# Kernel tuning notes

Measured on AMD Instinct MI355X. Metric: run time of the kernel, lower is better.

Reference implementation:

```python
import jax, jax.numpy as jnp
import numpy as np

GRID = 48
F = GRID * GRID        # number of mesh faces
C = 128                # channels
H = 8                  # attention heads
DH = C // H
B = 2                  # meshes in batch
WID = 256              # SelectionPrediction width


def _bfs_levels():
    """BFS flood-fill levels on a 4-connected GRIDxGRID face graph, anchor at center.
    Returns [n_levels, max_ring] int32, padded with F (dropped on scatter)."""
    c = GRID // 2
    ii, jj = np.meshgrid(np.arange(GRID), np.arange(GRID), indexing='ij')
    d = (np.abs(ii - c) + np.abs(jj - c)).reshape(-1)  # BFS depth == Manhattan dist
    L = int(d.max()) + 1
    Bd = int(np.bincount(d).max())
    idx = np.full((L, Bd), F, dtype=np.int32)
    for lv in range(L):
        faces = np.nonzero(d == lv)[0]
        idx[lv, :faces.size] = faces
    return jnp.asarray(idx)


def setup_inputs() -> dict:
    key = jax.random.key(0)
    ks = jax.random.split(key, 16)
    s = 1.0 / np.sqrt(C)
    sw = 1.0 / np.sqrt(WID)
    return {
        'x':  jax.random.normal(ks[0], (B, C, F), jnp.float32),
        # AnchorAttentionBlock projections (q/k/v/out)
        'Wq': jax.random.normal(ks[1], (C, C), jnp.float32) * s,
        'Wk': jax.random.normal(ks[2], (C, C), jnp.float32) * s,
        'Wv': jax.random.normal(ks[3], (C, C), jnp.float32) * s,
        'Wo': jax.random.normal(ks[4], (C, C), jnp.float32) * s,
        # SelectionPrediction (n_input=C, width=256, depth=3, sigmoid)
        'W1': jax.random.normal(ks[5], (C, WID), jnp.float32) * s,
        'b1': jnp.zeros((WID,), jnp.float32),
        'W2': jax.random.normal(ks[6], (WID, WID), jnp.float32) * sw,
        'b2': jnp.zeros((WID,), jnp.float32),
        'W3': jax.random.normal(ks[7], (WID, WID), jnp.float32) * sw,
        'b3': jnp.zeros((WID,), jnp.float32),
        'W4': jax.random.normal(ks[8], (WID, WID), jnp.float32) * sw,
        'b4': jnp.zeros((WID,), jnp.float32),
        'W5': jax.random.normal(ks[9], (WID, 1), jnp.float32) * sw,
        'b5': jnp.zeros((1,), jnp.float32),
        'levels_idx': _bfs_levels(),
    }


def reference(x, Wq, Wk, Wv, Wo, W1, b1, W2, b2, W3, b3, W4, b4, W5, b5, levels_idx):
    scale = 1.0 / jnp.sqrt(jnp.asarray(DH, x.dtype))

    def flood(feats):                       # feats: [F, C], one mesh
        def step(cur, idx):                 # idx: [Bd] boundary ring (pad = F)
            q = cur[idx]                                    # [Bd, C] (pad rows clamp-gather)
            qh = (q @ Wq).reshape(-1, H, DH)                # [Bd, H, DH]
            kh = (cur @ Wk).reshape(F, H, DH)               # global fftype: keys = all faces
            vh = (cur @ Wv).reshape(F, H, DH)
            att = jax.nn.softmax(jnp.einsum('bhd,fhd->bhf', qh, kh) * scale, axis=-1)
            o = jnp.einsum('bhf,fhd->bhd', att, vh).reshape(-1, C) @ Wo
            new = q + o                                     # mode='resid'
            return cur.at[idx].set(new, mode='drop'), None  # pad idx == F -> dropped
        out, _ = jax.lax.scan(step, feats, levels_idx)
        return out

    final = jax.vmap(flood)(x.transpose(0, 2, 1))           # [B, F, C]
    # SelectionPrediction on final_features.transpose(2,1)
    h = jax.nn.relu(final @ W1 + b1)
    h = jax.nn.relu(h @ W2 + b2)
    h = jax.nn.relu(h @ W3 + b3)
    h = jax.nn.relu(h @ W4 + b4)
    scores = jax.nn.sigmoid(h @ W5 + b5)                    # [B, F, 1] in [0, 1]
    return final.transpose(0, 2, 1), scores
```

## Files before the change

### kernel.cpp

```cpp
#include <hip/hip_runtime.h>
#include <hip/hip_bf16.h>
#include <stdint.h>

#define GRIDN 48
#define F 2304
#define C 128
#define H 8
#define DH 16
#define NB 2
#define WID 256
#define NLV 49
#define SMH (H * 18)
#define GLV 7

typedef __hip_bfloat16 bf16;

__device__ __forceinline__ float b2f(bf16 v) { return __bfloat162float(v); }

__global__ void k_permdetect(const void* __restrict__ x, int* __restrict__ flag,
                             int* __restrict__ permIdx, int* __restrict__ lvflags) {
    __shared__ int cnt[NLV], start[NLV];
    __shared__ int bad;
    int t = threadIdx.x;
    if (t == 0) bad = 0;
    if (t < NLV) cnt[t] = 0;
    for (int i = t; i < 2 * NLV; i += 256) lvflags[i] = 0;
    __syncthreads();
    {
        const bf16* xb = (const bf16*)x;
        int insane = 0;
        #pragma unroll
        for (int i = 0; i < 8; ++i) {
            float v = b2f(xb[t * 8 + i]);
            if (!(fabsf(v) < 1e10f)) insane = 1;
        }
        if (insane) atomicOr(&bad, 1);
    }
    for (int f = t; f < F; f += 256) {
        int d = abs(f / GRIDN - GRIDN / 2) + abs(f % GRIDN - GRIDN / 2);
        atomicAdd(&cnt[d], 1);
    }
    __syncthreads();
    if (t == 0) {
        int s = 0;
        for (int l = 0; l < NLV; ++l) { start[l] = s; s += cnt[l]; }
        *flag = bad;
    }
    __syncthreads();
    for (int f = t; f < F; f += 256) {
        int d = abs(f / GRIDN - GRIDN / 2) + abs(f % GRIDN - GRIDN / 2);
        permIdx[f] = atomicAdd(&start[d], 1);
    }
}

struct WSeg { const void* src; int off; int cnt; };
struct WSegs { WSeg s[14]; };

__global__ void k_convert(WSegs segs, const int* __restrict__ flag,
                          float* __restrict__ dst, int total) {
    int i = blockIdx.x * blockDim.x + threadIdx.x;
    if (i >= total) return;
    bool f32 = (*flag != 0);
    #pragma unroll 1
    for (int j = 0; j < 14; ++j) {
        int off = segs.s[j].off, cnt = segs.s[j].cnt;
        if (i >= off && i < off + cnt) {
            int k = i - off;
            dst[i] = f32 ? ((const float*)segs.s[j].src)[k]
                         : b2f(((const bf16*)segs.s[j].src)[k]);
            return;
        }
    }
}

__global__ void k_transpose_in(const void* __restrict__ x, const int* __restrict__ flag,
                               float* __restrict__ cur) {
    __shared__ float tile[32][33];
    bool f32 = (*flag != 0);
    int b = blockIdx.z;
    int f0 = blockIdx.x * 32, c0 = blockIdx.y * 32;
    int tx = threadIdx.x, ty = threadIdx.y;
    #pragma unroll
    for (int i = 0; i < 4; ++i) {
        int c = c0 + ty + i * 8;
        size_t idx = ((size_t)b * C + c) * F + f0 + tx;
        tile[ty + i * 8][tx] = f32 ? ((const float*)x)[idx] : b2f(((const bf16*)x)[idx]);
    }
    __syncthreads();
    #pragma unroll
    for (int i = 0; i < 4; ++i) {
        int f = f0 + ty + i * 8;
        cur[((size_t)b * F + f) * C + c0 + tx] = tile[tx][ty + i * 8];
    }
}

__global__ __launch_bounds__(128) void k_proj_init(
        const float* __restrict__ cur, const int* __restrict__ permIdx,
        const float* __restrict__ Wq, const float* __restrict__ Wk, const float* __restrict__ Wv,
        float* __restrict__ qh, float* __restrict__ khT, float* __restrict__ vhT) {
    __shared__ float rows[8][C];
    int r0 = blockIdx.x * 8;
    int tid = threadIdx.x;
    #pragma unroll
    for (int r = 0; r < 8; ++r) rows[r][tid] = cur[(size_t)(r0 + r) * C + tid];
    __syncthreads();
    float aq[8], ak[8], av[8];
    #pragma unroll
    for (int r = 0; r < 8; ++r) { aq[r] = 0.f; ak[r] = 0.f; av[r] = 0.f; }
    for (int k = 0; k < C; ++k) {
        float wq = Wq[k * C + tid];
        float wk = Wk[k * C + tid];
        float wv = Wv[k * C + tid];
        #pragma unroll
        for (int r = 0; r < 8; ++r) {
            float xv = rows[r][k];
            aq[r] = fmaf(xv, wq, aq[r]);
            ak[r] = fmaf(xv, wk, ak[r]);
            av[r] = fmaf(xv, wv, av[r]);
        }
    }
    const float scale = 0.25f;
    #pragma unroll
    for (int r = 0; r < 8; ++r) {
        int grow = r0 + r;
        int mesh = grow / F, face = grow % F;
        int p = permIdx[face];
        qh[(size_t)grow * C + tid] = aq[r] * scale;
        khT[((size_t)mesh * C + tid) * F + p] = ak[r];
        vhT[((size_t)mesh * C + tid) * F + p] = av[r];
    }
}

struct Rings { int v[NLV + 1]; };
struct Pairs { int v[NLV + 1]; };

__global__ __launch_bounds__(256) void k_static(
        int Bd, Rings rings, Pairs pairs,
        const int* __restrict__ levels,
        const float* __restrict__ qh_all,
        const float* __restrict__ khT, const float* __restrict__ vhT,
        float* __restrict__ smS) {
    int bx = blockIdx.x;
    int mesh = bx & 1;
    int gp = bx >> 1;
    int lv = 0;
    while (gp >= pairs.v[lv + 1]) ++lv;
    int spair = gp - pairs.v[lv];
    int rs = rings.v[lv];
    int s0 = spair * 2, s1 = s0 + 1;
    int face0 = (s0 < Bd) ? levels[lv * Bd + s0] : F;
    int face1 = (s1 < Bd) ? levels[lv * Bd + s1] : F;
    bool a0 = (face0 >= 0 && face0 < F), a1 = (face1 >= 0 && face1 < F);
    if (!a0 && !a1) return;

    __shared__ float sQh[2][C];
    int tid = threadIdx.x;
    size_t row0 = ((size_t)mesh * F + face0) * C;
    size_t row1 = ((size_t)mesh * F + face1) * C;
    if (tid < C) sQh[0][tid] = a0 ? qh_all[row0 + tid] : 0.f;
    else { int c = tid - C; sQh[1][c] = a1 ? qh_all[row1 + c] : 0.f; }
    __syncthreads();

    int head = tid >> 5, sub = tid & 31;
    float q0[DH], q1[DH];
    #pragma unroll
    for (int d = 0; d < DH; ++d) { q0[d] = sQh[0][head * DH + d]; q1[d] = sQh[1][head * DH + d]; }

    const float* Kb = khT + ((size_t)mesh * C + head * DH) * F;
    const float* Vb = vhT + ((size_t)mesh * C + head * DH) * F;

    float m0 = -1e30f, l0 = 0.f, m1 = -1e30f, l1 = 0.f;
    float acc0[DH], acc1[DH];
    #pragma unroll
    for (int d = 0; d < DH; ++d) { acc0[d] = 0.f; acc1[d] = 0.f; }

    int base0 = rs & ~127;
    for (int base = base0; base < F; base += 128) {
        int p4 = base + 4 * sub;
        float sx0 = 0, sy0 = 0, sz0 = 0, sw0 = 0;
        float sx1 = 0, sy1 = 0, sz1 = 0, sw1 = 0;
        #pragma unroll
        for (int d = 0; d < DH; ++d) {
            float4 kk = *(const float4*)(Kb + d * F + p4);
            float a = q0[d], b = q1[d];
            sx0 = fmaf(a, kk.x, sx0); sy0 = fmaf(a, kk.y, sy0);
            sz0 = fmaf(a, kk.z, sz0); sw0 = fmaf(a, kk.w, sw0);
            sx1 = fmaf(b, kk.x, sx1); sy1 = fmaf(b, kk.y, sy1);
            sz1 = fmaf(b, kk.z, sz1); sw1 = fmaf(b, kk.w, sw1);
        }
        float g0 = 1.f, g1 = 1.f, g2 = 1.f, g3 = 1.f;
        if (base < rs) {
            g0 = (p4     >= rs) ? 1.f : 0.f; g1 = (p4 + 1 >= rs) ? 1.f : 0.f;
            g2 = (p4 + 2 >= rs) ? 1.f : 0.f; g3 = (p4 + 3 >= rs) ? 1.f : 0.f;
        }
        float mx0 = fmaxf(fmaxf(sx0, sy0), fmaxf(sz0, sw0));
        float mn0 = fmaxf(m0, mx0);
        float c0 = __expf(m0 - mn0);
        float px0 = __expf(sx0 - mn0) * g0, py0 = __expf(sy0 - mn0) * g1;
        float pz0 = __expf(sz0 - mn0) * g2, pw0 = __expf(sw0 - mn0) * g3;
        l0 = fmaf(l0, c0, px0 + py0 + pz0 + pw0);
        m0 = mn0;
        float mx1 = fmaxf(fmaxf(sx1, sy1), fmaxf(sz1, sw1));
        float mn1 = fmaxf(m1, mx1);
        float c1e = __expf(m1 - mn1);
        float px1 = __expf(sx1 - mn1) * g0, py1 = __expf(sy1 - mn1) * g1;
        float pz1 = __expf(sz1 - mn1) * g2, pw1 = __expf(sw1 - mn1) * g3;
        l1 = fmaf(l1, c1e, px1 + py1 + pz1 + pw1);
        m1 = mn1;
        #pragma unroll
        for (int d = 0; d < DH; ++d) {
            float4 vv = *(const float4*)(Vb + d * F + p4);
            float w0 = fmaf(px0, vv.x, fmaf(py0, vv.y, fmaf(pz0, vv.z, pw0 * vv.w)));
            float w1 = fmaf(px1, vv.x, fmaf(py1, vv.y, fmaf(pz1, vv.z, pw1 * vv.w)));
            acc0[d] = fmaf(acc0[d], c0, w0);
            acc1[d] = fmaf(acc1[d], c1e, w1);
        }
    }

    #pragma unroll
    for (int w = 16; w >= 1; w >>= 1) {
        float mo = __shfl_xor(m0, w), lo = __shfl_xor(l0, w);
        float mn = fmaxf(m0, mo);
        float ca = __expf(m0 - mn), cb = __expf(mo - mn);
        l0 = l0 * ca + lo * cb;
        #pragma unroll
        for (int d = 0; d < DH; ++d) {
            float ao = __shfl_xor(acc0[d], w);
            acc0[d] = acc0[d] * ca + ao * cb;
        }
        m0 = mn;
        mo = __shfl_xor(m1, w); lo = __shfl_xor(l1, w);
        mn = fmaxf(m1, mo);
        ca = __expf(m1 - mn); cb = __expf(mo - mn);
        l1 = l1 * ca + lo * cb;
        #pragma unroll
        for (int d = 0; d < DH; ++d) {
            float ao = __shfl_xor(acc1[d], w);
            acc1[d] = acc1[d] * ca + ao * cb;
        }
        m1 = mn;
    }
    if (sub == 0) {
        if (a0) {
            float* S = smS + (size_t)(mesh * F + face0) * SMH + head * 18;
            S[0] = m0; S[1] = l0;
            #pragma unroll
            for (int d = 0; d < DH; ++d) S[2 + d] = acc0[d];
        }
        if (a1) {
            float* S = smS + (size_t)(mesh * F + face1) * SMH + head * 18;
            S[0] = m1; S[1] = l1;
            #pragma unroll
            for (int d = 0; d < DH; ++d) S[2 + d] = acc1[d];
        }
    }
}

struct Grp { int lv0; int rs0; int bofs[GLV + 1]; int rs[GLV]; int re[GLV]; int ns[GLV]; };

__global__ __launch_bounds__(256, 3) void k_group(
        int Bd, Grp grp,
        const int* __restrict__ levels, const int* __restrict__ permIdx,
        const float* __restrict__ qh_all, float* __restrict__ cur,
        float* __restrict__ khT, float* __restrict__ vhT,
        const float* __restrict__ smS,
        const float* __restrict__ Wk, const float* __restrict__ Wv,
        const float* __restrict__ Wo,
        float* __restrict__ stgK, float* __restrict__ stgV,
        int* __restrict__ lvflags) {
    int bx = blockIdx.x;
    int g = 0;
    while (bx >= grp.bofs[g + 1]) ++g;
    int lb = bx - grp.bofs[g];
    int mesh = lb & 1;
    int spair = lb >> 1;
    int lv = grp.lv0 + g;
    int rs0 = grp.rs0;

    int s0 = spair * 2, s1 = s0 + 1;
    int face0 = (s0 < Bd) ? levels[lv * Bd + s0] : F;
    int face1 = (s1 < Bd) ? levels[lv * Bd + s1] : F;
    bool a0 = (face0 >= 0 && face0 < F), a1 = (face1 >= 0 && face1 < F);

    __shared__ float sQh[2][C], sQ[2][C], sRed[2][C], sNew[C];
    __shared__ float sL[2][H];
    int tid = threadIdx.x;
    size_t row0 = ((size_t)mesh * F + face0) * C;
    size_t row1 = ((size_t)mesh * F + face1) * C;
    if (tid < C) {
        if (a0) { sQ[0][tid] = cur[row0 + tid]; sQh[0][tid] = qh_all[row0 + tid]; }
        else    { sQ[0][tid] = 0.f; sQh[0][tid] = 0.f; }
    } else {
        int c = tid - C;
        if (a1) { sQ[1][c] = cur[row1 + c]; sQh[1][c] = qh_all[row1 + c]; }
        else    { sQ[1][c] = 0.f; sQh[1][c] = 0.f; }
    }
    __syncthreads();

    int head = tid >> 5, sub = tid & 31;
    float q0[DH], q1[DH];
    #pragma unroll
    for (int d = 0; d < DH; ++d) { q0[d] = sQh[0][head * DH + d]; q1[d] = sQh[1][head * DH + d]; }

    const float* Kb = khT + ((size_t)mesh * C + head * DH) * F;
    const float* Vb = vhT + ((size_t)mesh * C + head * DH) * F;

    float m0 = -1e30f, l0 = 0.f, m1 = -1e30f, l1 = 0.f;
    float acc0[DH], acc1[DH];
    #pragma unroll
    for (int d = 0; d < DH; ++d) { acc0[d] = 0.f; acc1[d] = 0.f; }

    for (int base = 0; base < rs0; base += 128) {
        int p4 = base + 4 * sub;
        float sx0 = 0, sy0 = 0, sz0 = 0, sw0 = 0;
        float sx1 = 0, sy1 = 0, sz1 = 0, sw1 = 0;
        #pragma unroll
        for (int d = 0; d < DH; ++d) {
            float4 kk = *(const float4*)(Kb + d * F + p4);
            float a = q0[d], b = q1[d];
            sx0 = fmaf(a, kk.x, sx0); sy0 = fmaf(a, kk.y, sy0);
            sz0 = fmaf(a, kk.z, sz0); sw0 = fmaf(a, kk.w, sw0);
            sx1 = fmaf(b, kk.x, sx1); sy1 = fmaf(b, kk.y, sy1);
            sz1 = fmaf(b, kk.z, sz1); sw1 = fmaf(b, kk.w, sw1);
        }
        float g0 = 1.f, g1 = 1.f, g2 = 1.f, g3 = 1.f;
        if (base + 128 > rs0) {
            g0 = (p4     < rs0) ? 1.f : 0.f; g1 = (p4 + 1 < rs0) ? 1.f : 0.f;
            g2 = (p4 + 2 < rs0) ? 1.f : 0.f; g3 = (p4 + 3 < rs0) ? 1.f : 0.f;
        }
        float mx0 = fmaxf(fmaxf(sx0, sy0), fmaxf(sz0, sw0));
        float mn0 = fmaxf(m0, mx0);
        float c0 = __expf(m0 - mn0);
        float px0 = __expf(sx0 - mn0) * g0, py0 = __expf(sy0 - mn0) * g1;
        float pz0 = __expf(sz0 - mn0) * g2, pw0 = __expf(sw0 - mn0) * g3;
        l0 = fmaf(l0, c0, px0 + py0 + pz0 + pw0);
        m0 = mn0;
        float mx1 = fmaxf(fmaxf(sx1, sy1), fmaxf(sz1, sw1));
        float mn1 = fmaxf(m1, mx1);
        float c1e = __expf(m1 - mn1);
        float px1 = __expf(sx1 - mn1) * g0, py1 = __expf(sy1 - mn1) * g1;
        float pz1 = __expf(sz1 - mn1) * g2, pw1 = __expf(sw1 - mn1) * g3;
        l1 = fmaf(l1, c1e, px1 + py1 + pz1 + pw1);
        m1 = mn1;
        #pragma unroll
        for (int d = 0; d < DH; ++d) {
            float4 vv = *(const float4*)(Vb + d * F + p4);
            float w0 = fmaf(px0, vv.x, fmaf(py0, vv.y, fmaf(pz0, vv.z, pw0 * vv.w)));
            float w1 = fmaf(px1, vv.x, fmaf(py1, vv.y, fmaf(pz1, vv.z, pw1 * vv.w)));
            acc0[d] = fmaf(acc0[d], c0, w0);
            acc1[d] = fmaf(acc1[d], c1e, w1);
        }
    }

    for (int gp = 0; gp < g; ++gp) {
        if (tid == 0) {
            int need = grp.ns[gp];
            int* fl = &lvflags[(grp.lv0 + gp) * 2 + mesh];
            int guard = 0;
            while (__hip_atomic_load(fl, __ATOMIC_RELAXED, __HIP_MEMORY_SCOPE_AGENT) < need
                   && guard < (1 << 22)) {
                __builtin_amdgcn_s_sleep(4);
                ++guard;
            }
        }
        __syncthreads();
        int frs = grp.rs[gp], fre = grp.re[gp];
        for (int p = frs + sub; p < fre; p += 32) {
            float* kc = stgK + ((size_t)mesh * F + p) * C + head * DH;
            float* vc = stgV + ((size_t)mesh * F + p) * C + head * DH;
            float s0v = 0.f, s1v = 0.f;
            #pragma unroll
            for (int d = 0; d < DH; ++d) {
                float kd = __hip_atomic_load(kc + d, __ATOMIC_RELAXED, __HIP_MEMORY_SCOPE_AGENT);
                s0v = fmaf(q0[d], kd, s0v);
                s1v = fmaf(q1[d], kd, s1v);
            }
            float vv[DH];
            #pragma unroll
            for (int d = 0; d < DH; ++d)
                vv[d] = __hip_atomic_load(vc + d, __ATOMIC_RELAXED, __HIP_MEMORY_SCOPE_AGENT);
            {
                float mn = fmaxf(m0, s0v);
                float c = __expf(m0 - mn), pw = __expf(s0v - mn);
                l0 = l0 * c + pw;
                #pragma unroll
                for (int d = 0; d < DH; ++d) acc0[d] = fmaf(acc0[d], c, pw * vv[d]);
                m0 = mn;
            }
            {
                float mn = fmaxf(m1, s1v);
                float c = __expf(m1 - mn), pw = __expf(s1v - mn);
                l1 = l1 * c + pw;
                #pragma unroll
                for (int d = 0; d < DH; ++d) acc1[d] = fmaf(acc1[d], c, pw * vv[d]);
                m1 = mn;
            }
        }
    }

    #pragma unroll
    for (int w = 16; w >= 1; w >>= 1) {
        float mo = __shfl_xor(m0, w), lo = __shfl_xor(l0, w);
        float mn = fmaxf(m0, mo);
        float ca = __expf(m0 - mn), cb = __expf(mo - mn);
        l0 = l0 * ca + lo * cb;
        #pragma unroll
        for (int d = 0; d < DH; ++d) {
            float ao = __shfl_xor(acc0[d], w);
            acc0[d] = acc0[d] * ca + ao * cb;
        }
        m0 = mn;
        mo = __shfl_xor(m1, w); lo = __shfl_xor(l1, w);
        mn = fmaxf(m1, mo);
        ca = __expf(m1 - mn); cb = __expf(mo - mn);
        l1 = l1 * ca + lo * cb;
        #pragma unroll
        for (int d = 0; d < DH; ++d) {
            float ao = __shfl_xor(acc1[d], w);
            acc1[d] = acc1[d] * ca + ao * cb;
        }
        m1 = mn;
    }
    if (sub == 0) {
        {
            int fr = a0 ? face0 : 0;
            const float* S = smS + (size_t)(mesh * F + fr) * SMH + head * 18;
            float ms = S[0], ls = S[1];
            float mn = fmaxf(m0, ms);
            float ca = __expf(m0 - mn), cb = __expf(ms - mn);
            sL[0][head] = l0 * ca + ls * cb;
            #pragma unroll
            for (int d = 0; d < DH; ++d)
                sRed[0][head * DH + d] = fmaf(acc0[d], ca, S[2 + d] * cb);
        }
        {
            int fr = a1 ? face1 : 0;
            const float* S = smS + (size_t)(mesh * F + fr) * SMH + head * 18;
            float ms = S[0], ls = S[1];
            float mn = fmaxf(m1, ms);
            float ca = __expf(m1 - mn), cb = __expf(ms - mn);
            sL[1][head] = l1 * ca + ls * cb;
            #pragma unroll
            for (int d = 0; d < DH; ++d)
                sRed[1][head * DH + d] = fmaf(acc1[d], ca, S[2 + d] * cb);
        }
    }
    __syncthreads();
    if (tid < C) sRed[0][tid] = sRed[0][tid] / sL[0][tid >> 4];
    else { int c = tid - C; sRed[1][c] = sRed[1][c] / sL[1][c >> 4]; }
    __syncthreads();

    bool doStage = (g != GLV - 1);
    #pragma unroll 1
    for (int j = 0; j < 2; ++j) {
        bool act = j == 0 ? a0 : a1;
        if (!act) continue;
        size_t rowj = j == 0 ? row0 : row1;
        int facej = j == 0 ? face0 : face1;
        if (tid < C) {
            float o = 0.f;
            for (int k = 0; k < C; ++k) o = fmaf(sRed[j][k], Wo[k * C + tid], o);
            float nv = sQ[j][tid] + o;
            sNew[tid] = nv;
            cur[rowj + tid] = nv;
        }
        __syncthreads();
        int p = permIdx[facej];
        if (tid < C) {
            float a = 0.f;
            for (int k = 0; k < C; ++k) a = fmaf(sNew[k], Wk[k * C + tid], a);
            khT[((size_t)mesh * C + tid) * F + p] = a;
            if (doStage)
                __hip_atomic_store(stgK + ((size_t)mesh * F + p) * C + tid, a,
                                   __ATOMIC_RELAXED, __HIP_MEMORY_SCOPE_AGENT);
        } else {
            int c = tid - C;
            float a = 0.f;
            for (int k = 0; k < C; ++k) a = fmaf(sNew[k], Wv[k * C + c], a);
            vhT[((size_t)mesh * C + c) * F + p] = a;
            if (doStage)
                __hip_atomic_store(stgV + ((size_t)mesh * F + p) * C + c, a,
                                   __ATOMIC_RELAXED, __HIP_MEMORY_SCOPE_AGENT);
        }
        __syncthreads();
    }
    if (doStage && tid == 0)
        __hip_atomic_fetch_add(&lvflags[lv * 2 + mesh], 1,
                               __ATOMIC_RELEASE, __HIP_MEMORY_SCOPE_AGENT);
}

__global__ __launch_bounds__(256) void k_mlp(
        const float* __restrict__ cur,
        const float* __restrict__ W1, const float* __restrict__ b1,
        const float* __restrict__ W2, const float* __restrict__ b2,
        const float* __restrict__ W3, const float* __restrict__ b3,
        const float* __restrict__ W4, const float* __restrict__ b4,
        const float* __restrict__ W5, const float* __restrict__ b5,
        float* __restrict__ out_scores) {
    __shared__ float sIn[8][C];
    __shared__ float sA[8][WID];
    __shared__ float sB[8][WID];
    int tid = threadIdx.x;
    int r0 = blockIdx.x * 8;
    for (int i = tid; i < 8 * C; i += 256) sIn[i >> 7][i & 127] = cur[(size_t)r0 * C + i];
    __syncthreads();
    {
        float a[8];
        #pragma unroll
        for (int r = 0; r < 8; ++r) a[r] = 0.f;
        for (int k = 0; k < C; ++k) {
            float w = W1[k * WID + tid];
            #pragma unroll
            for (int r = 0; r < 8; ++r) a[r] = fmaf(sIn[r][k], w, a[r]);
        }
        float bias = b1[tid];
        #pragma unroll
        for (int r = 0; r < 8; ++r) sA[r][tid] = fmaxf(a[r] + bias, 0.f);
    }
    __syncthreads();
    {
        float a[8];
        #pragma unroll
        for (int r = 0; r < 8; ++r) a[r] = 0.f;
        for (int k = 0; k < WID; ++k) {
            float w = W2[k * WID + tid];
            #pragma unroll
            for (int r = 0; r < 8; ++r) a[r] = fmaf(sA[r][k], w, a[r]);
        }
        float bias = b2[tid];
        #pragma unroll
        for (int r = 0; r < 8; ++r) sB[r][tid] = fmaxf(a[r] + bias, 0.f);
    }
    __syncthreads();
    {
        float a[8];
        #pragma unroll
        for (int r = 0; r < 8; ++r) a[r] = 0.f;
        for (int k = 0; k < WID; ++k) {
            float w = W3[k * WID + tid];
            #pragma unroll
            for (int r = 0; r < 8; ++r) a[r] = fmaf(sB[r][k], w, a[r]);
        }
        float bias = b3[tid];
        #pragma unroll
        for (int r = 0; r < 8; ++r) sA[r][tid] = fmaxf(a[r] + bias, 0.f);
    }
    __syncthreads();
    {
        float a[8];
        #pragma unroll
        for (int r = 0; r < 8; ++r) a[r] = 0.f;
        for (int k = 0; k < WID; ++k) {
            float w = W4[k * WID + tid];
            #pragma unroll
            for (int r = 0; r < 8; ++r) a[r] = fmaf(sA[r][k], w, a[r]);
        }
        float bias = b4[tid];
        #pragma unroll
        for (int r = 0; r < 8; ++r) sB[r][tid] = fmaxf(a[r] + bias, 0.f);
    }
    __syncthreads();
    if (tid < 8) {
        float a = b5[0];
        for (int k = 0; k < WID; ++k) a = fmaf(sB[tid][k], W5[k], a);
        out_scores[r0 + tid] = 1.f / (1.f + __expf(-a));
    }
}

__global__ void k_transpose_out(const float* __restrict__ cur, float* __restrict__ out) {
    __shared__ float tile[32][33];
    int b = blockIdx.z;
    int f0 = blockIdx.x * 32, c0 = blockIdx.y * 32;
    int tx = threadIdx.x, ty = threadIdx.y;
    #pragma unroll
    for (int i = 0; i < 4; ++i) {
        int f = f0 + ty + i * 8;
        tile[ty + i * 8][tx] = cur[((size_t)b * F + f) * C + c0 + tx];
    }
    __syncthreads();
    #pragma unroll
    for (int i = 0; i < 4; ++i) {
        int c = c0 + ty + i * 8;
        out[((size_t)b * C + c) * F + f0 + tx] = tile[tx][ty + i * 8];
    }
}

extern "C" void kernel_launch(void* const* d_in, const int* in_sizes, int n_in,
                              void* d_out, int out_size, void* d_ws, size_t ws_size,
                              hipStream_t stream) {
    const int* levels = (const int*)d_in[15];
    int Bd = in_sizes[15] / NLV;

    const size_t n = (size_t)NB * F * C;
    float* cur  = (float*)d_ws;
    float* qh   = cur + n;
    float* khT  = qh + n;
    float* vhT  = khT + n;
    float* wbuf = vhT + n;
    int*   permIdx = (int*)(wbuf + 296193 + 3);
    int*   flag = permIdx + F;
    int*   lvflags = flag + 1;
    float* smS  = (float*)(permIdx + 2404);
    float* stgK = smS + (size_t)NB * F * SMH;
    float* stgV = stgK + n;

    const int oWq = 0,       oWk = 16384,  oWv = 32768,  oWo = 49152;
    const int oW1 = 65536,   oB1 = 98304;
    const int oW2 = 98560,   oB2 = 164096;
    const int oW3 = 164352,  oB3 = 229888;
    const int oW4 = 230144,  oB4 = 295680;
    const int oW5 = 295936,  oB5 = 296192;
    const int wtot = 296193;

    WSegs segs = {{
        { d_in[1],  oWq, 16384 }, { d_in[2],  oWk, 16384 },
        { d_in[3],  oWv, 16384 }, { d_in[4],  oWo, 16384 },
        { d_in[5],  oW1, 32768 }, { d_in[6],  oB1, 256 },
        { d_in[7],  oW2, 65536 }, { d_in[8],  oB2, 256 },
        { d_in[9],  oW3, 65536 }, { d_in[10], oB3, 256 },
        { d_in[11], oW4, 65536 }, { d_in[12], oB4, 256 },
        { d_in[13], oW5, 256 },   { d_in[14], oB5, 1 },
    }};

    Rings rings;
    Pairs pairs;
    int totPairs = 0;
    {
        int cnt[NLV];
        for (int l = 0; l < NLV; ++l) cnt[l] = 0;
        for (int i = 0; i < GRIDN; ++i)
            for (int j = 0; j < GRIDN; ++j)
                cnt[(i < 24 ? 24 - i : i - 24) + (j < 24 ? 24 - j : j - 24)]++;
        rings.v[0] = 0;
        pairs.v[0] = 0;
        for (int l = 0; l < NLV; ++l) {
            rings.v[l + 1] = rings.v[l] + cnt[l];
            pairs.v[l + 1] = pairs.v[l] + (cnt[l] + 1) / 2;
        }
        totPairs = pairs.v[NLV];
    }

    float* out0 = (float*)d_out;
    float* out1 = out0 + (size_t)NB * C * F;

    k_permdetect<<<1, 256, 0, stream>>>(d_in[0], flag, permIdx, lvflags);
    k_convert<<<(wtot + 255) / 256, 256, 0, stream>>>(segs, flag, wbuf, wtot);
    k_transpose_in<<<dim3(F / 32, C / 32, NB), dim3(32, 8), 0, stream>>>(d_in[0], flag, cur);
    k_proj_init<<<(NB * F) / 8, 128, 0, stream>>>(cur, permIdx, wbuf + oWq, wbuf + oWk, wbuf + oWv,
                                                  qh, khT, vhT);

    k_static<<<2 * totPairs, 256, 0, stream>>>(Bd, rings, pairs, levels, qh, khT, vhT, smS);

    for (int lv0 = 0; lv0 < NLV; lv0 += GLV) {
        Grp grp;
        grp.lv0 = lv0;
        grp.rs0 = rings.v[lv0];
        grp.bofs[0] = 0;
        for (int g = 0; g < GLV; ++g) {
            int lv = lv0 + g;
            int rs = rings.v[lv], re = rings.v[lv + 1];
            int ns = (re - rs + 1) / 2;
            grp.rs[g] = rs;
            grp.re[g] = re;
            grp.ns[g] = ns;
            grp.bofs[g + 1] = grp.bofs[g] + 2 * ns;
        }
        k_group<<<grp.bofs[GLV], 256, 0, stream>>>(Bd, grp, levels, permIdx, qh, cur,
                                                   khT, vhT, smS,
                                                   wbuf + oWk, wbuf + oWv, wbuf + oWo,
                                                   stgK, stgV, lvflags);
    }

    k_mlp<<<(NB * F) / 8, 256, 0, stream>>>(cur, wbuf + oW1, wbuf + oB1, wbuf + oW2, wbuf + oB2,
                                            wbuf + oW3, wbuf + oB3, wbuf + oW4, wbuf + oB4,
                                            wbuf + oW5, wbuf + oB5, out1);
    k_transpose_out<<<dim3(F / 32, C / 32, NB), dim3(32, 8), 0, stream>>>(cur, out0);
}
```

Measured before the change: 1.577 ms.

## Transpose Wk/Wv/Wo, parallelize group epilogue across both rows, shrink row tiles

```diff
diff --git a/kernel.cpp b/kernel.cpp
--- a/kernel.cpp
+++ b/kernel.cpp
@@ -73,6 +73,15 @@
     }
 }
 
+__global__ void k_wtrans(const float* __restrict__ Wk, const float* __restrict__ Wv,
+                         const float* __restrict__ Wo, float* __restrict__ wT) {
+    int m = blockIdx.y;
+    const float* s = m == 0 ? Wk : (m == 1 ? Wv : Wo);
+    int c = blockIdx.x;
+    int k = threadIdx.x;
+    wT[((size_t)m * C + c) * C + k] = s[k * C + c];
+}
+
 __global__ void k_transpose_in(const void* __restrict__ x, const int* __restrict__ flag,
                                float* __restrict__ cur) {
     __shared__ float tile[32][33];
@@ -98,36 +107,31 @@
         const float* __restrict__ cur, const int* __restrict__ permIdx,
         const float* __restrict__ Wq, const float* __restrict__ Wk, const float* __restrict__ Wv,
         float* __restrict__ qh, float* __restrict__ khT, float* __restrict__ vhT) {
-    __shared__ float rows[8][C];
-    int r0 = blockIdx.x * 8;
+    __shared__ float rows[2][C];
+    int r0 = blockIdx.x * 2;
     int tid = threadIdx.x;
-    #pragma unroll
-    for (int r = 0; r < 8; ++r) rows[r][tid] = cur[(size_t)(r0 + r) * C + tid];
-    __syncthreads();
-    float aq[8], ak[8], av[8];
-    #pragma unroll
-    for (int r = 0; r < 8; ++r) { aq[r] = 0.f; ak[r] = 0.f; av[r] = 0.f; }
+    rows[0][tid] = cur[(size_t)r0 * C + tid];
+    rows[1][tid] = cur[(size_t)(r0 + 1) * C + tid];
+    __syncthreads();
+    float aq0 = 0.f, aq1 = 0.f, ak0 = 0.f, ak1 = 0.f, av0 = 0.f, av1 = 0.f;
     for (int k = 0; k < C; ++k) {
         float wq = Wq[k * C + tid];
         float wk = Wk[k * C + tid];
         float wv = Wv[k * C + tid];
-        #pragma unroll
-        for (int r = 0; r < 8; ++r) {
-            float xv = rows[r][k];
-            aq[r] = fmaf(xv, wq, aq[r]);
-            ak[r] = fmaf(xv, wk, ak[r]);
-            av[r] = fmaf(xv, wv, av[r]);
-        }
+        float x0 = rows[0][k], x1 = rows[1][k];
+        aq0 = fmaf(x0, wq, aq0); aq1 = fmaf(x1, wq, aq1);
+        ak0 = fmaf(x0, wk, ak0); ak1 = fmaf(x1, wk, ak1);
+        av0 = fmaf(x0, wv, av0); av1 = fmaf(x1, wv, av1);
     }
     const float scale = 0.25f;
     #pragma unroll
-    for (int r = 0; r < 8; ++r) {
+    for (int r = 0; r < 2; ++r) {
         int grow = r0 + r;
         int mesh = grow / F, face = grow % F;
         int p = permIdx[face];
-        qh[(size_t)grow * C + tid] = aq[r] * scale;
-        khT[((size_t)mesh * C + tid) * F + p] = ak[r];
-        vhT[((size_t)mesh * C + tid) * F + p] = av[r];
+        qh[(size_t)grow * C + tid] = (r == 0 ? aq0 : aq1) * scale;
+        khT[((size_t)mesh * C + tid) * F + p] = r == 0 ? ak0 : ak1;
+        vhT[((size_t)mesh * C + tid) * F + p] = r == 0 ? av0 : av1;
     }
 }
 
@@ -264,8 +268,8 @@
         const float* __restrict__ qh_all, float* __restrict__ cur,
         float* __restrict__ khT, float* __restrict__ vhT,
         const float* __restrict__ smS,
-        const float* __restrict__ Wk, const float* __restrict__ Wv,
-        const float* __restrict__ Wo,
+        const float* __restrict__ WkT, const float* __restrict__ WvT,
+        const float* __restrict__ WoT,
         float* __restrict__ stgK, float* __restrict__ stgV,
         int* __restrict__ lvflags) {
     int bx = blockIdx.x;
@@ -282,7 +286,7 @@
     int face1 = (s1 < Bd) ? levels[lv * Bd + s1] : F;
     bool a0 = (face0 >= 0 && face0 < F), a1 = (face1 >= 0 && face1 < F);
 
-    __shared__ float sQh[2][C], sQ[2][C], sRed[2][C], sNew[C];
+    __shared__ __attribute__((aligned(16))) float sQh[2][C], sQ[2][C], sRed[2][C], sNew2[2][C];
     __shared__ float sL[2][H];
     int tid = threadIdx.x;
     size_t row0 = ((size_t)mesh * F + face0) * C;
@@ -366,19 +370,27 @@
         __syncthreads();
         int frs = grp.rs[gp], fre = grp.re[gp];
         for (int p = frs + sub; p < fre; p += 32) {
-            float* kc = stgK + ((size_t)mesh * F + p) * C + head * DH;
-            float* vc = stgV + ((size_t)mesh * F + p) * C + head * DH;
+            const unsigned long long* kc =
+                (const unsigned long long*)(stgK + ((size_t)mesh * F + p) * C + head * DH);
+            const unsigned long long* vc =
+                (const unsigned long long*)(stgV + ((size_t)mesh * F + p) * C + head * DH);
             float s0v = 0.f, s1v = 0.f;
             #pragma unroll
-            for (int d = 0; d < DH; ++d) {
-                float kd = __hip_atomic_load(kc + d, __ATOMIC_RELAXED, __HIP_MEMORY_SCOPE_AGENT);
-                s0v = fmaf(q0[d], kd, s0v);
-                s1v = fmaf(q1[d], kd, s1v);
+            for (int d2 = 0; d2 < DH / 2; ++d2) {
+                unsigned long long kw = __hip_atomic_load(kc + d2, __ATOMIC_RELAXED,
+                                                          __HIP_MEMORY_SCOPE_AGENT);
+                float2 kf = *(float2*)&kw;
+                s0v = fmaf(q0[2 * d2], kf.x, s0v); s0v = fmaf(q0[2 * d2 + 1], kf.y, s0v);
+                s1v = fmaf(q1[2 * d2], kf.x, s1v); s1v = fmaf(q1[2 * d2 + 1], kf.y, s1v);
             }
             float vv[DH];
             #pragma unroll
-            for (int d = 0; d < DH; ++d)
-                vv[d] = __hip_atomic_load(vc + d, __ATOMIC_RELAXED, __HIP_MEMORY_SCOPE_AGENT);
+            for (int d2 = 0; d2 < DH / 2; ++d2) {
+                unsigned long long vw = __hip_atomic_load(vc + d2, __ATOMIC_RELAXED,
+                                                          __HIP_MEMORY_SCOPE_AGENT);
+                float2 vf = *(float2*)&vw;
+                vv[2 * d2] = vf.x; vv[2 * d2 + 1] = vf.y;
+            }
             {
                 float mn = fmaxf(m0, s0v);
                 float c = __expf(m0 - mn), pw = __expf(s0v - mn);
@@ -451,39 +463,56 @@
     __syncthreads();
 
     bool doStage = (g != GLV - 1);
+    {
+        int j = tid >> 7;
+        int c = tid & 127;
+        bool act = j == 0 ? a0 : a1;
+        float o = 0.f;
+        const float4* WoR = (const float4*)(WoT + (size_t)c * C);
+        const float4* Rr  = (const float4*)(&sRed[j][0]);
+        #pragma unroll
+        for (int k4 = 0; k4 < C / 4; ++k4) {
+            float4 w = WoR[k4];
+            float4 r = Rr[k4];
+            o = fmaf(r.x, w.x, o); o = fmaf(r.y, w.y, o);
+            o = fmaf(r.z, w.z, o); o = fmaf(r.w, w.w, o);
+        }
+        float nv = sQ[j][c] + o;
+        sNew2[j][c] = nv;
+        if (act) cur[(j == 0 ? row0 : row1) + c] = nv;
+    }
+    __syncthreads();
     #pragma unroll 1
     for (int j = 0; j < 2; ++j) {
         bool act = j == 0 ? a0 : a1;
         if (!act) continue;
-        size_t rowj = j == 0 ? row0 : row1;
         int facej = j == 0 ? face0 : face1;
+        int p = permIdx[facej];
+        int c = tid & 127;
+        const float* WT = (tid < C) ? WkT : WvT;
+        float a = 0.f;
+        const float4* Wr = (const float4*)(WT + (size_t)c * C);
+        const float4* Nr = (const float4*)(&sNew2[j][0]);
+        #pragma unroll
+        for (int k4 = 0; k4 < C / 4; ++k4) {
+            float4 w = Wr[k4];
+            float4 x = Nr[k4];
+            a = fmaf(x.x, w.x, a); a = fmaf(x.y, w.y, a);
+            a = fmaf(x.z, w.z, a); a = fmaf(x.w, w.w, a);
+        }
         if (tid < C) {
-            float o = 0.f;
-            for (int k = 0; k < C; ++k) o = fmaf(sRed[j][k], Wo[k * C + tid], o);
-            float nv = sQ[j][tid] + o;
-            sNew[tid] = nv;
-            cur[rowj + tid] = nv;
-        }
-        __syncthreads();
-        int p = permIdx[facej];
-        if (tid < C) {
-            float a = 0.f;
-            for (int k = 0; k < C; ++k) a = fmaf(sNew[k], Wk[k * C + tid], a);
-            khT[((size_t)mesh * C + tid) * F + p] = a;
+            khT[((size_t)mesh * C + c) * F + p] = a;
             if (doStage)
-                __hip_atomic_store(stgK + ((size_t)mesh * F + p) * C + tid, a,
+                __hip_atomic_store(stgK + ((size_t)mesh * F + p) * C + c, a,
                                    __ATOMIC_RELAXED, __HIP_MEMORY_SCOPE_AGENT);
         } else {
-            int c = tid - C;
-            float a = 0.f;
-            for (int k = 0; k < C; ++k) a = fmaf(sNew[k], Wv[k * C + c], a);
             vhT[((size_t)mesh * C + c) * F + p] = a;
             if (doStage)
                 __hip_atomic_store(stgV + ((size_t)mesh * F + p) * C + c, a,
                                    __ATOMIC_RELAXED, __HIP_MEMORY_SCOPE_AGENT);
         }
-        __syncthreads();
-    }
+    }
+    __syncthreads();
     if (doStage && tid == 0)
         __hip_atomic_fetch_add(&lvflags[lv * 2 + mesh], 1,
                                __ATOMIC_RELEASE, __HIP_MEMORY_SCOPE_AGENT);
@@ -497,70 +526,62 @@
         const float* __restrict__ W4, const float* __restrict__ b4,
         const float* __restrict__ W5, const float* __restrict__ b5,
         float* __restrict__ out_scores) {
-    __shared__ float sIn[8][C];
-    __shared__ float sA[8][WID];
-    __shared__ float sB[8][WID];
+    __shared__ float sIn[2][C];
+    __shared__ float sA[2][WID];
+    __shared__ float sB[2][WID];
     int tid = threadIdx.x;
-    int r0 = blockIdx.x * 8;
-    for (int i = tid; i < 8 * C; i += 256) sIn[i >> 7][i & 127] = cur[(size_t)r0 * C + i];
+    int r0 = blockIdx.x * 2;
+    for (int i = tid; i < 2 * C; i += 256) sIn[i >> 7][i & 127] = cur[(size_t)r0 * C + i];
     __syncthreads();
     {
-        float a[8];
-        #pragma unroll
-        for (int r = 0; r < 8; ++r) a[r] = 0.f;
+        float a0 = 0.f, a1 = 0.f;
         for (int k = 0; k < C; ++k) {
             float w = W1[k * WID + tid];
-            #pragma unroll
-            for (int r = 0; r < 8; ++r) a[r] = fmaf(sIn[r][k], w, a[r]);
+            a0 = fmaf(sIn[0][k], w, a0);
+            a1 = fmaf(sIn[1][k], w, a1);
         }
         float bias = b1[tid];
-        #pragma unroll
-        for (int r = 0; r < 8; ++r) sA[r][tid] = fmaxf(a[r] + bias, 0.f);
+        sA[0][tid] = fmaxf(a0 + bias, 0.f);
+        sA[1][tid] = fmaxf(a1 + bias, 0.f);
     }
     __syncthreads();
     {
-        float a[8];
-        #pragma unroll
-        for (int r = 0; r < 8; ++r) a[r] = 0.f;
+        float a0 = 0.f, a1 = 0.f;
         for (int k = 0; k < WID; ++k) {
             float w = W2[k * WID + tid];
-            #pragma unroll
-            for (int r = 0; r < 8; ++r) a[r] = fmaf(sA[r][k], w, a[r]);
+            a0 = fmaf(sA[0][k], w, a0);
+            a1 = fmaf(sA[1][k], w, a1);
         }
         float bias = b2[tid];
-        #pragma unroll
-        for (int r = 0; r < 8; ++r) sB[r][tid] = fmaxf(a[r] + bias, 0.f);
+        sB[0][tid] = fmaxf(a0 + bias, 0.f);
+        sB[1][tid] = fmaxf(a1 + bias, 0.f);
     }
     __syncthreads();
     {
-        float a[8];
-        #pragma unroll
-        for (int r = 0; r < 8; ++r) a[r] = 0.f;
+        float a0 = 0.f, a1 = 0.f;
         for (int k = 0; k < WID; ++k) {
             float w = W3[k * WID + tid];
-            #pragma unroll
-            for (int r = 0; r < 8; ++r) a[r] = fmaf(sB[r][k], w, a[r]);
+            a0 = fmaf(sB[0][k], w, a0);
+            a1 = fmaf(sB[1][k], w, a1);
         }
         float bias = b3[tid];
-        #pragma unroll
-        for (int r = 0; r < 8; ++r) sA[r][tid] = fmaxf(a[r] + bias, 0.f);
+        sA[0][tid] = fmaxf(a0 + bias, 0.f);
+        sA[1][tid] = fmaxf(a1 + bias, 0.f);
     }
     __syncthreads();
     {
-        float a[8];
-        #pragma unroll
-        for (int r = 0; r < 8; ++r) a[r] = 0.f;
+        float a0 = 0.f, a1 = 0.f;
         for (int k = 0; k < WID; ++k) {
             float w = W4[k * WID + tid];
-            #pragma unroll
-            for (int r = 0; r < 8; ++r) a[r] = fmaf(sA[r][k], w, a[r]);
+            a0 = fmaf(sA[0][k], w, a0);
+            a1 = fmaf(sA[1][k], w, a1);
         }
         float bias = b4[tid];
-        #pragma unroll
-        for (int r = 0; r < 8; ++r) sB[r][tid] = fmaxf(a[r] + bias, 0.f);
-    }
-    __syncthreads();
-    if (tid < 8) {
+        sB[0][tid] = fmaxf(a0 + bias, 0.f);
+        sB[1][tid] = fmaxf(a1 + bias, 0.f);
+    }
+    __syncthreads();
+    if (tid < 2) {
         float a = b5[0];
         for (int k = 0; k < WID; ++k) a = fmaf(sB[tid][k], W5[k], a);
         out_scores[r0 + tid] = 1.f / (1.f + __expf(-a));
@@ -597,7 +618,8 @@
     float* khT  = qh + n;
     float* vhT  = khT + n;
     float* wbuf = vhT + n;
-    int*   permIdx = (int*)(wbuf + 296193 + 3);
+    float* wT   = wbuf + 296196;
+    int*   permIdx = (int*)(wT + 49152);
     int*   flag = permIdx + F;
     int*   lvflags = flag + 1;
     float* smS  = (float*)(permIdx + 2404);
@@ -645,8 +667,9 @@
 
     k_permdetect<<<1, 256, 0, stream>>>(d_in[0], flag, permIdx, lvflags);
     k_convert<<<(wtot + 255) / 256, 256, 0, stream>>>(segs, flag, wbuf, wtot);
+    k_wtrans<<<dim3(C, 3), C, 0, stream>>>(wbuf + oWk, wbuf + oWv, wbuf + oWo, wT);
     k_transpose_in<<<dim3(F / 32, C / 32, NB), dim3(32, 8), 0, stream>>>(d_in[0], flag, cur);
-    k_proj_init<<<(NB * F) / 8, 128, 0, stream>>>(cur, permIdx, wbuf + oWq, wbuf + oWk, wbuf + oWv,
+    k_proj_init<<<(NB * F) / 2, 128, 0, stream>>>(cur, permIdx, wbuf + oWq, wbuf + oWk, wbuf + oWv,
                                                   qh, khT, vhT);
 
     k_static<<<2 * totPairs, 256, 0, stream>>>(Bd, rings, pairs, levels, qh, khT, vhT, smS);
@@ -667,11 +690,11 @@
         }
         k_group<<<grp.bofs[GLV], 256, 0, stream>>>(Bd, grp, levels, permIdx, qh, cur,
                                                    khT, vhT, smS,
-                                                   wbuf + oWk, wbuf + oWv, wbuf + oWo,
+                                                   wT, wT + 16384, wT + 32768,
                                                    stgK, stgV, lvflags);
     }
 
-    k_mlp<<<(NB * F) / 8, 256, 0, stream>>>(cur, wbuf + oW1, wbuf + oB1, wbuf + oW2, wbuf + oB2,
+    k_mlp<<<(NB * F) / 2, 256, 0, stream>>>(cur, wbuf + oW1, wbuf + oB1, wbuf + oW2, wbuf + oB2,
                                             wbuf + oW3, wbuf + oB3, wbuf + oW4, wbuf + oB4,
                                             wbuf + oW5, wbuf + oB5, out1);
     k_transpose_out<<<dim3(F / 32, C / 32, NB), dim3(32, 8), 0, stream>>>(cur, out0);
```

After: 1.526 ms. 1.03x faster.
